# Performance work log

Measured on AMD Instinct MI355X. Metric: run time of the kernel, lower is better.

## Reference

```python
import jax, jax.numpy as jnp
import numpy as np

EPS = 0.05  # mesh.epsilon boundary band


def _pool_one(adj, image, vs, edges):
    # adj: [N,N] bool, image: [N,F] f32, vs: [N,2] f32 in [0,1], edges: [2,E] int32
    N, F = image.shape
    E = edges.shape[1]
    K = N // 2                      # out_target
    tgt_kills = N - K               # number of vertices removed
    v0, v1 = edges[0], edges[1]
    # heap key = sum of squares of concat(image[v0], image[v1])
    cost = jnp.sum(image[v0] * image[v0], -1) + jnp.sum(image[v1] * image[v1], -1)
    def bnd(p):
        return (p[:, 0] < EPS) | (p[:, 0] > 1 - EPS) | (p[:, 1] < EPS) | (p[:, 1] > 1 - EPS)
    ok = ~(bnd(vs[v0]) | bnd(vs[v1]))   # boundary_mask = ~is_boundary
    # heappop of [value, id] lists == stable sort by cost (ties broken by edge id)
    order = jnp.argsort(cost)
    # sequential greedy collapse: kill v1 if edge interior and both endpoints alive
    def step(carry, eid):
        mask, nk = carry
        a, b = v0[eid], v1[eid]
        acc = ok[eid] & mask[a] & mask[b] & (nk < tgt_kills)
        mask = mask.at[b].set(mask[b] & ~acc)
        return (mask, nk + acc.astype(jnp.int32)), acc
    (mask, _), accepts = jax.lax.scan(step, (jnp.ones(N, bool), jnp.int32(0)), order)
    sv0, sv1 = v0[order], v1[order]
    # mapping m: dead vertex -> absorbing vertex (identity elsewhere)
    dead = jnp.where(accepts, sv1, N)          # N = out-of-range -> dropped
    m = jnp.arange(N).at[dead].set(sv0, mode='drop')
    # update_matrix: scatter-add collapsed vertex features into absorber rows
    upd = jnp.zeros_like(image).at[jnp.where(accepts, sv0, N)].add(image[sv1], mode='drop')
    image2 = image + upd
    # merge_vertex on adjacency: union rows then columns of merged vertices
    A = adj.astype(jnp.uint8)
    A1 = jnp.zeros_like(A).at[m].max(A)        # merge rows
    A2 = jnp.zeros_like(A1).at[m].max(A1.T).T  # merge cols
    alive = jnp.nonzero(mask, size=K, fill_value=0)[0]  # exactly K survivors
    adj_out = A2[alive][:, alive].astype(bool) & ~jnp.eye(K, dtype=bool)
    return adj_out, image2[alive]


def setup_inputs() -> dict:
    key = jax.random.key(0)
    k1, k2, k3, k4, k5 = jax.random.split(key, 5)
    B, N, F, E = 4, 8192, 64, 65536
    adj = jax.random.bernoulli(k1, 0.002, (B, N, N))
    image = jax.random.normal(k2, (B, N, F), jnp.float32)
    vs = jax.random.uniform(k3, (B, N, 2), dtype=jnp.float32)
    a = jax.random.randint(k4, (B, 1, E), 0, N)
    off = jax.random.randint(k5, (B, 1, E), 1, N)
    b = (a + off) % N                           # guarantee v0 != v1
    edges = jnp.concatenate([a, b], axis=1).astype(jnp.int32)
    return {"adj": adj, "image": image, "vs": vs, "edges": edges}


def reference(adj, image, vs, edges):
    # returns (pooled adjacency [B,N//2,N//2] bool, pooled features [B,N//2,F])
    return jax.vmap(_pool_one)(adj, image, vs, edges)
```

## Files before the change

kernel.cpp:

```cpp
#include <hip/hip_runtime.h>
#include <stdint.h>

typedef unsigned long long u64;
typedef unsigned int u32;
typedef unsigned char u8;

#define Bn 4
#define Nv 8192
#define Fd 64
#define Ed 65536
#define Kv 4096
#define TGTK 4096
#define NW 256
#define QB 4096
#define BCAP 256

#define WS_FLAGS   ((size_t)0)
#define WS_ACCCNT  ((size_t)256)
#define WS_FB      ((size_t)512)
#define WS_MM      ((size_t)768)
#define WS_HIST    ((size_t)4096)
#define WS_CTR     (WS_HIST + (size_t)Bn*QB*4)
#define WS_OUTBITS (WS_CTR + (size_t)Bn*QB*4)
#define WS_ZERO_BYTES (WS_OUTBITS + (size_t)Bn*Kv*128*4)
#define WS_OFF     (WS_ZERO_BYTES)
#define WS_KFULL   (WS_OFF + (size_t)Bn*4104*4)
#define WS_PACK    (WS_KFULL + (size_t)Bn*Ed*8)
#define WS_BKEY    (WS_PACK + (size_t)Bn*Ed*4)
#define WS_BPK     (WS_BKEY + (size_t)Bn*Ed*8)
#define WS_SPACK   (WS_BPK + (size_t)Bn*Ed*4)
#define WS_SQ      (WS_SPACK + (size_t)Bn*Ed*4)
#define WS_BND     (WS_SQ + (size_t)Bn*Nv*4)
#define WS_MAP     (WS_BND + (size_t)Bn*Nv)
#define WS_POS     (WS_MAP + (size_t)Bn*Nv*4)
#define WS_PM      (WS_POS + (size_t)Bn*Nv*4)
#define WS_ALIVEW  (WS_PM + (size_t)Bn*Nv*4)
#define WS_ALIST   (WS_ALIVEW + (size_t)Bn*NW*4)
#define WS_ACC     (WS_ALIST + (size_t)Bn*Kv*4)

__global__ void k_vertex(const u8* adj, u32* flags, const float* image, const float* vs,
                         float* sq, u8* bnd, int* map) {
#pragma clang fp contract(off)
    int idx = blockIdx.x * 256 + threadIdx.x;
    const float* row = image + (size_t)idx * Fd;
    float r[8];
#pragma unroll
    for (int j = 0; j < 8; ++j) r[j] = row[j] * row[j];
#pragma unroll
    for (int i = 8; i < 64; i += 8)
#pragma unroll
        for (int j = 0; j < 8; ++j) r[j] += row[i + j] * row[i + j];
    float s = ((r[0] + r[1]) + (r[2] + r[3])) + ((r[4] + r[5]) + (r[6] + r[7]));
    sq[idx] = s;
    float x = vs[(size_t)idx * 2], y = vs[(size_t)idx * 2 + 1];
    const float LO = 0.05f;
    const float HI = (float)(1.0 - 0.05);
    bnd[idx] = ((x < LO) || (x > HI) || (y < LO) || (y > HI)) ? 1 : 0;
    map[idx] = idx & (Nv - 1);
    const u32* w = (const u32*)adj;
    bool f0 = false, f1 = false, f2 = false, f3 = false;
    for (int i = idx; i < (1 << 19); i += 32768) {
        u32 v = w[i];
        f0 |= (v & 0x000000FFu) != 0;
        f1 |= (v & 0x0000FF00u) != 0;
        f2 |= (v & 0x00FF0000u) != 0;
        f3 |= (v & 0xFF000000u) != 0;
    }
    u32 m = 0;
    if (__ballot(f0)) m |= 1;
    if (__ballot(f1)) m |= 2;
    if (__ballot(f2)) m |= 4;
    if (__ballot(f3)) m |= 8;
    if ((threadIdx.x & 63) == 0 && m) atomicOr(flags, m);
}

__global__ void k_edge(const int* edges, const float* sq, const u8* bnd,
                       u64* kfull, u32* pack, u32* mm) {
    int idx = blockIdx.x * 256 + threadIdx.x;
    if (idx >= Bn * Ed) return;
    int b = idx >> 16, e = idx & (Ed - 1);
    int v0 = edges[(size_t)b * 2 * Ed + e];
    int v1 = edges[(size_t)b * 2 * Ed + Ed + e];
    float c = sq[b * Nv + v0] + sq[b * Nv + v1];
    u32 cb = __float_as_uint(c);
    kfull[idx] = ((u64)cb << 16) | (u32)e;
    u32 okk = (!bnd[b * Nv + v0] && !bnd[b * Nv + v1]) ? 1u : 0u;
    pack[idx] = (u32)v0 | ((u32)v1 << 13) | (okk << 26);
    u32 mn = cb, mx = cb;
#pragma unroll
    for (int o = 32; o; o >>= 1) {
        u32 a = (u32)__shfl_xor((int)mn, o);
        u32 d = (u32)__shfl_xor((int)mx, o);
        mn = mn < a ? mn : a;
        mx = mx > d ? mx : d;
    }
    if ((threadIdx.x & 63) == 0) {
        atomicMax(&mm[b * 2], ~mn);
        atomicMax(&mm[b * 2 + 1], mx);
    }
}

__device__ __forceinline__ int qbin(u32 cb, u32 mm0, u32 mm1) {
    float minC = __uint_as_float(~mm0);
    float maxC = __uint_as_float(mm1);
    float span = maxC - minC;
    float scale = (float)QB / (span > 1e-30f ? span : 1e-30f);
    int bin = (int)((__uint_as_float(cb) - minC) * scale);
    return bin < 0 ? 0 : (bin > QB - 1 ? QB - 1 : bin);
}

__global__ __launch_bounds__(256) void k_qhist(const u64* kfull, const u32* mm, u32* hist) {
    __shared__ u32 lh[QB];
    int tid = threadIdx.x;
    for (int i = tid; i < QB; i += 256) lh[i] = 0;
    __syncthreads();
    size_t base = (size_t)blockIdx.x * 2048;
    int b = (int)(base >> 16);
    u32 mm0 = mm[b * 2], mm1 = mm[b * 2 + 1];
#pragma unroll
    for (int r = 0; r < 8; ++r) {
        u32 cb = (u32)(kfull[base + r * 256 + tid] >> 16);
        atomicAdd(&lh[qbin(cb, mm0, mm1)], 1u);
    }
    __syncthreads();
    for (int i = tid; i < QB; i += 256) {
        u32 v = lh[i];
        if (v) atomicAdd(&hist[b * QB + i], v);
    }
}

__global__ __launch_bounds__(1024) void k_qscan(const u32* hist, u32* off) {
    int b = blockIdx.x, tid = threadIdx.x;
    const u32* h = hist + b * QB;
    u32 h4[4];
    u32 s = 0;
#pragma unroll
    for (int q = 0; q < 4; ++q) { h4[q] = h[tid * 4 + q]; s += h4[q]; }
    __shared__ u32 sc[1024];
    sc[tid] = s;
    __syncthreads();
    for (int o = 1; o < 1024; o <<= 1) {
        u32 t = (tid >= o) ? sc[tid - o] : 0u;
        __syncthreads();
        sc[tid] += t;
        __syncthreads();
    }
    u32 run = sc[tid] - s;
    u32* ob = off + b * 4104;
#pragma unroll
    for (int q = 0; q < 4; ++q) { ob[tid * 4 + q] = run; run += h4[q]; }
    if (tid == 1023) ob[QB] = sc[1023];
}

__global__ void k_qscat(const u64* kfull, const u32* pack, const u32* mm, const u32* off,
                        u32* ctr, u64* bkey, u32* bpk) {
    int idx = blockIdx.x * 256 + threadIdx.x;
    if (idx >= Bn * Ed) return;
    int b = idx >> 16;
    u64 kf = kfull[idx];
    u32 cb = (u32)(kf >> 16);
    u32 e = (u32)(kf & 0xFFFFu);
    int bin = qbin(cb, mm[b * 2], mm[b * 2 + 1]);
    u32 slot = atomicAdd(&ctr[b * QB + bin], 1u);
    u32 dst = off[b * 4104 + bin] + slot;
    bkey[(size_t)b * Ed + dst] = ((u64)cb << 24) | ((u64)e << 8) | (u64)(slot & 255u);
    bpk[(size_t)b * Ed + dst] = pack[idx];
}

__global__ __launch_bounds__(256) void k_qsort(const u64* bkey, const u32* bpk, const u32* off,
                                               u32* spack, u32* fb) {
    __shared__ u64 sk[4][BCAP];
    int wave = threadIdx.x >> 6, lane = threadIdx.x & 63;
    int b = blockIdx.x >> 10;
    int bin = (blockIdx.x & 1023) * 4 + wave;
    u32 start = off[b * 4104 + bin];
    u32 end = off[b * 4104 + bin + 1];
    int len = (int)(end - start);
    bool okbin = (len > 0 && len <= BCAP);
    const u64* kb = bkey + (size_t)b * Ed + start;
    for (int i = lane; i < BCAP; i += 64)
        sk[wave][i] = (okbin && i < len) ? kb[i] : ~0ull;
    if (len > BCAP && lane == 0) atomicOr(fb, 1u);
    __syncthreads();
    for (int k = 2; k <= BCAP; k <<= 1) {
        for (int j = k >> 1; j > 0; j >>= 1) {
#pragma unroll
            for (int t = lane; t < BCAP / 2; t += 64) {
                int i = ((t & ~(j - 1)) << 1) | (t & (j - 1));
                bool asc = ((i & k) == 0);
                u64 a = sk[wave][i], c = sk[wave][i | j];
                if ((a > c) == asc) { sk[wave][i] = c; sk[wave][i | j] = a; }
            }
            __syncthreads();
        }
    }
    if (okbin) {
        const u32* pb = bpk + (size_t)b * Ed + start;
        u32* so = spack + (size_t)b * Ed + start;
        for (int r = lane; r < len; r += 64) {
            u32 s = (u32)(sk[wave][r] & 255u);
            so[r] = pb[s];
        }
    }
}

__global__ __launch_bounds__(1024) void k_sortFB(u64* kfull, const u32* pack, u32* spack,
                                                 const u32* fb) {
    if (*fb == 0) return;
    int b = blockIdx.x;
    u64* kb = kfull + (size_t)b * Ed;
    __shared__ u64 s[8192];
    int tid = threadIdx.x;
    for (int ch = 0; ch < 8; ++ch) {
        u64* cb = kb + ch * 8192;
        int gb = ch * 8192;
        for (int p = 0; p < 8; ++p) s[p * 1024 + tid] = cb[p * 1024 + tid];
        __syncthreads();
        for (int k = 2; k <= 8192; k <<= 1)
            for (int j = k >> 1; j > 0; j >>= 1) {
                for (int p = 0; p < 4; ++p) {
                    int t = p * 1024 + tid;
                    int i = ((t & ~(j - 1)) << 1) | (t & (j - 1));
                    bool asc = (((gb + i) & k) == 0);
                    u64 a = s[i], c = s[i | j];
                    if ((a > c) == asc) { s[i] = c; s[i | j] = a; }
                }
                __syncthreads();
            }
        for (int p = 0; p < 8; ++p) cb[p * 1024 + tid] = s[p * 1024 + tid];
        __syncthreads();
    }
    for (int k = 16384; k <= 65536; k <<= 1) {
        for (int j = k >> 1; j >= 8192; j >>= 1) {
            for (int p = 0; p < 32; ++p) {
                int t = p * 1024 + tid;
                int i = ((t & ~(j - 1)) << 1) | (t & (j - 1));
                bool asc = ((i & k) == 0);
                u64 a = kb[i], c = kb[i | j];
                if ((a > c) == asc) { kb[i] = c; kb[i | j] = a; }
            }
            __syncthreads();
        }
        for (int ch = 0; ch < 8; ++ch) {
            u64* cb = kb + ch * 8192;
            bool asc = (((ch * 8192) & k) == 0);
            for (int p = 0; p < 8; ++p) s[p * 1024 + tid] = cb[p * 1024 + tid];
            __syncthreads();
            for (int j = 4096; j > 0; j >>= 1) {
                for (int p = 0; p < 4; ++p) {
                    int t = p * 1024 + tid;
                    int i = ((t & ~(j - 1)) << 1) | (t & (j - 1));
                    u64 a = s[i], c = s[i | j];
                    if ((a > c) == asc) { s[i] = c; s[i | j] = a; }
                }
                __syncthreads();
            }
            for (int p = 0; p < 8; ++p) cb[p * 1024 + tid] = s[p * 1024 + tid];
            __syncthreads();
        }
    }
    for (int i = tid; i < Ed; i += 1024)
        spack[(size_t)b * Ed + i] = pack[(size_t)b * Ed + (u32)(kb[i] & 0xFFFFu)];
}

__global__ __launch_bounds__(64) void k_greedy(const u32* spack, int* map, u32* aliveW,
                                               int* accList, u32* accCnt) {
    int b = blockIdx.x;
    int lane = threadIdx.x;
    __shared__ u32 alive[NW];
    __shared__ u32 mlane[Nv];
    for (int i = lane; i < NW; i += 64) alive[i] = 0xFFFFFFFFu;
    for (int i = lane; i < Nv; i += 64) mlane[i] = 64u;
    const u32* sp = spack + (size_t)b * Ed;
    u32 pc = sp[lane];
    __syncthreads();
    int nk = 0;
    const int G = Ed / 64;
    for (int g = 0; g < G; ++g) {
        u32 pn = (g + 1 < G) ? sp[(g + 1) * 64 + lane] : 0u;
        int v0 = pc & 8191;
        int v1 = (pc >> 13) & 8191;
        bool okk = (pc >> 26) & 1u;
        bool a0 = (alive[v0 >> 5] >> (v0 & 31)) & 1u;
        bool a1 = (alive[v1 >> 5] >> (v1 & 31)) & 1u;
        bool spec = okk && a0 && a1;
        if (spec) atomicMin(&mlane[v1], (u32)lane);
        __syncthreads();
        bool conf = false;
        if (spec) conf = (mlane[v0] < (u32)lane) || (mlane[v1] < (u32)lane);
        u64 specM = __ballot(spec);
        u64 confM = __ballot(conf);
        u64 accM = specM & ~confM;
        u64 rem = confM;
        while (rem) {
            int l = __ffsll((unsigned long long)rem) - 1;
            rem &= rem - 1;
            int bv0 = __shfl(v0, l);
            int bv1 = __shfl(v1, l);
            bool killer = ((accM >> lane) & 1ull) && (lane < l) && (v1 == bv0 || v1 == bv1);
            if (__ballot(killer) == 0ull) accM |= 1ull << l;
        }
        int cnt = __popcll(accM);
        int remK = TGTK - nk;
        bool acc = (accM >> lane) & 1ull;
        if (cnt > remK) {
            int rr = __popcll(accM & ((1ull << lane) - 1ull));
            if (acc && rr >= remK) acc = false;
            accM = __ballot(acc);
            cnt = remK;
        }
        if (acc) {
            atomicAnd(&alive[v1 >> 5], ~(1u << (v1 & 31)));
            map[(size_t)b * Nv + v1] = v0;
            int rr = __popcll(accM & ((1ull << lane) - 1ull));
            int slot = nk + rr;
            accList[((size_t)b * TGTK + slot) * 2] = v0;
            accList[((size_t)b * TGTK + slot) * 2 + 1] = v1;
        }
        if (spec) mlane[v1] = 64u;
        nk += cnt;
        __syncthreads();
        if (nk >= TGTK) break;
        pc = pn;
    }
    for (int i = lane; i < NW; i += 64) aliveW[b * NW + i] = alive[i];
    if (lane == 0) accCnt[b] = (u32)nk;
}

__global__ __launch_bounds__(256) void k_scan(const u32* aliveW, const int* map,
                                              int* pos, int* pm, int* alist) {
    int b = blockIdx.x, tid = threadIdx.x;
    __shared__ u32 cnt[256];
    __shared__ u32 off[256];
    u32 w = aliveW[b * NW + tid];
    cnt[tid] = __popc(w);
    __syncthreads();
    if (tid == 0) { u32 s = 0; for (int i = 0; i < 256; ++i) { off[i] = s; s += cnt[i]; } }
    __syncthreads();
    u32 base = off[tid];
    int* posb = pos + (size_t)b * Nv;
    int* alb = alist + (size_t)b * Kv;
    for (int bit = 0; bit < 32; ++bit) {
        int v = tid * 32 + bit;
        int p = -1;
        if ((w >> bit) & 1u) {
            if (base < Kv) { p = (int)base; alb[base] = v; }
            base++;
        }
        posb[v] = p;
    }
    __syncthreads();
    const int* mapb = map + (size_t)b * Nv;
    int* pmb = pm + (size_t)b * Nv;
    for (int v = tid; v < Nv; v += 256) pmb[v] = posb[mapb[v]];
}

__global__ void k_fcopy(const float* image, const int* alist, float* outF) {
    int idx = blockIdx.x * 256 + threadIdx.x;
    if (idx >= Bn * Kv * 16) return;
    int b = idx >> 16, r = idx & 65535;
    int x = r >> 4, f4 = r & 15;
    int src = alist[b * Kv + x];
    const float4* s = (const float4*)(image + ((size_t)(b * Nv + src)) * Fd) + f4;
    float4* d = (float4*)(outF + ((size_t)(b * Kv + x)) * Fd) + f4;
    *d = *s;
}

__global__ __launch_bounds__(64) void k_fscat(const float* image, const int* accList,
                                              const u32* accCnt, const int* pos, float* outF) {
    int b = blockIdx.x >> 12, e = blockIdx.x & 4095;
    if (e >= (int)accCnt[b]) return;
    int v0 = accList[((size_t)b * TGTK + e) * 2];
    int v1 = accList[((size_t)b * TGTK + e) * 2 + 1];
    int x = pos[(size_t)b * Nv + v0];
    if (x < 0) return;
    int f = threadIdx.x;
    atomicAdd(outF + ((size_t)(b * Kv + x)) * Fd + f,
              image[((size_t)(b * Nv + v1)) * Fd + f]);
}

__global__ __launch_bounds__(256) void k_merge(const u8* adj, const u32* flags,
                                               const int* pm, u32* outbits) {
    int bi = blockIdx.x;
    int b = bi >> 13, i = bi & (Nv - 1);
    int t = pm[(size_t)b * Nv + i];
    if (t < 0) return;
    __shared__ u32 bits[Kv / 32];
    int tid = threadIdx.x;
    if (tid < 128) bits[tid] = 0;
    __syncthreads();
    const int* pmb = pm + (size_t)b * Nv;
    u32 fw = flags[0];
    bool bytefmt = (fw & 1) && (fw & 8);
    auto put = [&](int col) {
        int c = pmb[col];
        if (c >= 0) atomicOr(&bits[c >> 5], 1u << (c & 31));
    };
    if (bytefmt) {
        const uint4* row = (const uint4*)(adj + ((size_t)b * Nv + i) * Nv);
#pragma unroll
        for (int it = 0; it < 2; ++it) {
            uint4 v = row[it * 256 + tid];
            if (v.x | v.y | v.z | v.w) {
                int cb = (it * 256 + tid) * 16;
                u32 wv[4] = { v.x, v.y, v.z, v.w };
                for (int q = 0; q < 4; ++q) {
                    u32 u = wv[q];
                    if (!u) continue;
#pragma unroll
                    for (int kk = 0; kk < 4; ++kk)
                        if ((u >> (8 * kk)) & 0xFFu) put(cb + q * 4 + kk);
                }
            }
        }
    } else {
        const uint4* row = (const uint4*)((const u32*)adj + ((size_t)b * Nv + i) * Nv);
        for (int it = 0; it < 8; ++it) {
            uint4 v = row[it * 256 + tid];
            int cb = (it * 256 + tid) * 4;
            if (v.x) put(cb);
            if (v.y) put(cb + 1);
            if (v.z) put(cb + 2);
            if (v.w) put(cb + 3);
        }
    }
    __syncthreads();
    if (tid < 128) {
        u32 bw = bits[tid];
        if (bw) atomicOr(&outbits[((size_t)b * Kv + t) * 128 + tid], bw);
    }
}

__global__ void k_expand(const u32* outbits, float* out) {
    int idx = blockIdx.x;
    int tid = threadIdx.x;
    int b = idx >> 14, r = idx & 16383;
    int x = r >> 2, seg = r & 3;
    int c0 = seg * 1024 + tid * 4;
    u32 w = outbits[((size_t)b * Kv + x) * 128 + (c0 >> 5)];
    u32 nib = (w >> (c0 & 31)) & 0xFu;
    float4 f;
    f.x = (nib & 1) ? 1.f : 0.f;
    f.y = (nib & 2) ? 1.f : 0.f;
    f.z = (nib & 4) ? 1.f : 0.f;
    f.w = (nib & 8) ? 1.f : 0.f;
    if (x >= c0 && x < c0 + 4) ((float*)&f)[x - c0] = 0.f;
    *((float4*)(out + ((size_t)(b * Kv + x)) * Kv + c0)) = f;
}

extern "C" void kernel_launch(void* const* d_in, const int* in_sizes, int n_in,
                              void* d_out, int out_size, void* d_ws, size_t ws_size,
                              hipStream_t stream) {
    const u8* adj = (const u8*)d_in[0];
    const float* image = (const float*)d_in[1];
    const float* vs = (const float*)d_in[2];
    const int* edges = (const int*)d_in[3];
    char* ws = (char*)d_ws;
    u32* flags = (u32*)(ws + WS_FLAGS);
    u32* accCnt = (u32*)(ws + WS_ACCCNT);
    u32* fb = (u32*)(ws + WS_FB);
    u32* mm = (u32*)(ws + WS_MM);
    u32* hist = (u32*)(ws + WS_HIST);
    u32* ctr = (u32*)(ws + WS_CTR);
    u32* outbits = (u32*)(ws + WS_OUTBITS);
    u32* off = (u32*)(ws + WS_OFF);
    u64* kfull = (u64*)(ws + WS_KFULL);
    u32* pack = (u32*)(ws + WS_PACK);
    u64* bkey = (u64*)(ws + WS_BKEY);
    u32* bpk = (u32*)(ws + WS_BPK);
    u32* spack = (u32*)(ws + WS_SPACK);
    float* sq = (float*)(ws + WS_SQ);
    u8* bnd = (u8*)(ws + WS_BND);
    int* map = (int*)(ws + WS_MAP);
    int* pos = (int*)(ws + WS_POS);
    int* pm = (int*)(ws + WS_PM);
    u32* aliveW = (u32*)(ws + WS_ALIVEW);
    int* alist = (int*)(ws + WS_ALIST);
    int* accList = (int*)(ws + WS_ACC);
    float* outA = (float*)d_out;
    float* outF = outA + (size_t)Bn * Kv * Kv;

    hipMemsetAsync(d_ws, 0, WS_ZERO_BYTES, stream);
    k_vertex<<<Bn * Nv / 256, 256, 0, stream>>>(adj, flags, image, vs, sq, bnd, map);
    k_edge<<<Bn * Ed / 256, 256, 0, stream>>>(edges, sq, bnd, kfull, pack, mm);
    k_qhist<<<Bn * Ed / 2048, 256, 0, stream>>>(kfull, mm, hist);
    k_qscan<<<Bn, 1024, 0, stream>>>(hist, off);
    k_qscat<<<Bn * Ed / 256, 256, 0, stream>>>(kfull, pack, mm, off, ctr, bkey, bpk);
    k_qsort<<<Bn * 1024, 256, 0, stream>>>(bkey, bpk, off, spack, fb);
    k_sortFB<<<Bn, 1024, 0, stream>>>(kfull, pack, spack, fb);
    k_greedy<<<Bn, 64, 0, stream>>>(spack, map, aliveW, accList, accCnt);
    k_scan<<<Bn, 256, 0, stream>>>(aliveW, map, pos, pm, alist);
    k_fcopy<<<Bn * Kv * 16 / 256, 256, 0, stream>>>(image, alist, outF);
    k_fscat<<<Bn * TGTK, 64, 0, stream>>>(image, accList, accCnt, pos, outF);
    k_merge<<<Bn * Nv, 256, 0, stream>>>(adj, flags, pm, outbits);
    k_expand<<<Bn * Kv * 4, 256, 0, stream>>>(outbits, outA);
}
```

Measured before the change: 2.064 ms.

## Fuse outbits zeroing into scatter, size bin sorts to length, use wave barriers

Moves the zeroing of the 8 MB outbits bitmap out of the up-front memset and into k_qscat, where each thread writes two uint4 zeros. In k_qsort, each wave now sorts only up to the next power of two above its bin length rather than always 256 entries. It returns early on empty or oversized bins and uses wave barriers instead of block-wide barriers. k_greedy, which runs as a single wave, also swaps __syncthreads for wave barriers. The changes rely on each wave owning its own shared-memory slice, and on LDS ordering within a wave being enough for correctness.

```diff
diff --git a/kernel.cpp b/kernel.cpp
--- a/kernel.cpp
+++ b/kernel.cpp
@@ -21,9 +21,9 @@
 #define WS_MM      ((size_t)768)
 #define WS_HIST    ((size_t)4096)
 #define WS_CTR     (WS_HIST + (size_t)Bn*QB*4)
-#define WS_OUTBITS (WS_CTR + (size_t)Bn*QB*4)
-#define WS_ZERO_BYTES (WS_OUTBITS + (size_t)Bn*Kv*128*4)
-#define WS_OFF     (WS_ZERO_BYTES)
+#define WS_ZERO_BYTES (WS_CTR + (size_t)Bn*QB*4)
+#define WS_OUTBITS (WS_ZERO_BYTES)
+#define WS_OFF     (WS_OUTBITS + (size_t)Bn*Kv*128*4)
 #define WS_KFULL   (WS_OFF + (size_t)Bn*4104*4)
 #define WS_PACK    (WS_KFULL + (size_t)Bn*Ed*8)
 #define WS_BKEY    (WS_PACK + (size_t)Bn*Ed*4)
@@ -153,9 +153,12 @@
 }
 
 __global__ void k_qscat(const u64* kfull, const u32* pack, const u32* mm, const u32* off,
-                        u32* ctr, u64* bkey, u32* bpk) {
+                        u32* ctr, u64* bkey, u32* bpk, uint4* outbits4) {
     int idx = blockIdx.x * 256 + threadIdx.x;
     if (idx >= Bn * Ed) return;
+    uint4 z = make_uint4(0, 0, 0, 0);
+#pragma unroll
+    for (int q = 0; q < 2; ++q) outbits4[(size_t)q * Bn * Ed + idx] = z;
     int b = idx >> 16;
     u64 kf = kfull[idx];
     u32 cb = (u32)(kf >> 16);
@@ -176,31 +179,30 @@
     u32 start = off[b * 4104 + bin];
     u32 end = off[b * 4104 + bin + 1];
     int len = (int)(end - start);
-    bool okbin = (len > 0 && len <= BCAP);
+    if (len <= 0) return;
+    if (len > BCAP) { if (lane == 0) atomicOr(fb, 1u); return; }
+    int m = 2;
+    while (m < len) m <<= 1;
     const u64* kb = bkey + (size_t)b * Ed + start;
-    for (int i = lane; i < BCAP; i += 64)
-        sk[wave][i] = (okbin && i < len) ? kb[i] : ~0ull;
-    if (len > BCAP && lane == 0) atomicOr(fb, 1u);
-    __syncthreads();
-    for (int k = 2; k <= BCAP; k <<= 1) {
+    u64* s = sk[wave];
+    for (int i = lane; i < m; i += 64) s[i] = (i < len) ? kb[i] : ~0ull;
+    __builtin_amdgcn_wave_barrier();
+    for (int k = 2; k <= m; k <<= 1) {
         for (int j = k >> 1; j > 0; j >>= 1) {
-#pragma unroll
-            for (int t = lane; t < BCAP / 2; t += 64) {
+            for (int t = lane; t < (m >> 1); t += 64) {
                 int i = ((t & ~(j - 1)) << 1) | (t & (j - 1));
                 bool asc = ((i & k) == 0);
-                u64 a = sk[wave][i], c = sk[wave][i | j];
-                if ((a > c) == asc) { sk[wave][i] = c; sk[wave][i | j] = a; }
+                u64 a = s[i], c = s[i | j];
+                if ((a > c) == asc) { s[i] = c; s[i | j] = a; }
             }
-            __syncthreads();
-        }
-    }
-    if (okbin) {
-        const u32* pb = bpk + (size_t)b * Ed + start;
-        u32* so = spack + (size_t)b * Ed + start;
-        for (int r = lane; r < len; r += 64) {
-            u32 s = (u32)(sk[wave][r] & 255u);
-            so[r] = pb[s];
-        }
+            __builtin_amdgcn_wave_barrier();
+        }
+    }
+    const u32* pb = bpk + (size_t)b * Ed + start;
+    u32* so = spack + (size_t)b * Ed + start;
+    for (int r = lane; r < len; r += 64) {
+        u32 sl = (u32)(s[r] & 255u);
+        so[r] = pb[sl];
     }
 }
 
@@ -273,7 +275,7 @@
     for (int i = lane; i < Nv; i += 64) mlane[i] = 64u;
     const u32* sp = spack + (size_t)b * Ed;
     u32 pc = sp[lane];
-    __syncthreads();
+    __builtin_amdgcn_wave_barrier();
     int nk = 0;
     const int G = Ed / 64;
     for (int g = 0; g < G; ++g) {
@@ -285,7 +287,7 @@
         bool a1 = (alive[v1 >> 5] >> (v1 & 31)) & 1u;
         bool spec = okk && a0 && a1;
         if (spec) atomicMin(&mlane[v1], (u32)lane);
-        __syncthreads();
+        __builtin_amdgcn_wave_barrier();
         bool conf = false;
         if (spec) conf = (mlane[v0] < (u32)lane) || (mlane[v1] < (u32)lane);
         u64 specM = __ballot(spec);
@@ -319,7 +321,7 @@
         }
         if (spec) mlane[v1] = 64u;
         nk += cnt;
-        __syncthreads();
+        __builtin_amdgcn_wave_barrier();
         if (nk >= TGTK) break;
         pc = pn;
     }
@@ -485,7 +487,8 @@
     k_edge<<<Bn * Ed / 256, 256, 0, stream>>>(edges, sq, bnd, kfull, pack, mm);
     k_qhist<<<Bn * Ed / 2048, 256, 0, stream>>>(kfull, mm, hist);
     k_qscan<<<Bn, 1024, 0, stream>>>(hist, off);
-    k_qscat<<<Bn * Ed / 256, 256, 0, stream>>>(kfull, pack, mm, off, ctr, bkey, bpk);
+    k_qscat<<<Bn * Ed / 256, 256, 0, stream>>>(kfull, pack, mm, off, ctr, bkey, bpk,
+                                               (uint4*)outbits);
     k_qsort<<<Bn * 1024, 256, 0, stream>>>(bkey, bpk, off, spack, fb);
     k_sortFB<<<Bn, 1024, 0, stream>>>(kfull, pack, spack, fb);
     k_greedy<<<Bn, 64, 0, stream>>>(spack, map, aliveW, accList, accCnt);
```

New measurement: 2.024 ms. Within noise of the previous version (-1.9%).
